# Performance work log

Measured on AMD Instinct MI355X. Metric: run time of the kernel, lower is better.

## Reference

```python
import jax, jax.numpy as jnp
import numpy as np

FP8_MAX = 448.0  # e4m3fn saturation value

def q8(x):
    """Round-to-nearest-even quantization to float8 e4m3fn values (kept in fp32).
    Normal min exponent -6, mantissa 3 bits, subnormal step 2^-9, saturate at 448."""
    a = jnp.abs(x)
    e = jnp.clip(jnp.floor(jnp.log2(jnp.maximum(a, 1e-30))), -6.0, 8.0)
    step = jnp.exp2(e - 3.0)  # mantissa quantization step for this binade
    q = jnp.minimum(jnp.round(a / step) * step, FP8_MAX)  # jnp.round is half-to-even
    return jnp.sign(x) * q

def setup_inputs() -> dict:
    key = jax.random.key(0)
    k1, k2, k3 = jax.random.split(key, 3)
    B, D_IN, D_H, D_OUT = 8192, 1024, 4096, 1024
    x = jax.random.normal(k1, (B, D_IN), jnp.float32)
    # learned weights (torch Linear layout: [out, in]); scaled to a realistic FP8 range
    w1 = jax.random.normal(k2, (D_H, D_IN), jnp.float32) * 0.03
    w2 = jax.random.normal(k3, (D_OUT, D_H), jnp.float32) * 0.03
    return {"x": x, "w1": w1, "w2": w2}

def reference(x, w1, w2):
    # x -> fp8 e4m3fn -> bit-pulse encode (lossless round trip for fp8 values)
    x8 = q8(x)
    # spike FP8 linear layers carry fp8 weights (set_weight_from_float quantizes)
    w1q = q8(w1)
    w2q = q8(w2)
    # fc1: spike spatial-encoding adder == accumulate wide, emit FP8 pulses
    h = q8(jnp.einsum('bi,hi->bh', x8, w1q))
    # SpikeFP8ReLU: zero out negative fp8 pulse values
    h = jnp.where(h > 0, h, 0.0)
    # fc2 then fp8_bits_to_float decode
    out = q8(jnp.einsum('bh,oh->bo', h, w2q))
    return out
```

## Files before the change

kernel.cpp:

```cpp
#include <hip/hip_runtime.h>
#include <stdint.h>
#include <stddef.h>

typedef int v4i  __attribute__((ext_vector_type(4)));
typedef int v16i __attribute__((ext_vector_type(16)));

#define KCH  256
#define BUFB (128 * 256)
#define LDSB (2 * BUFB)

__device__ __forceinline__ void gl_lds16(const uint8_t* g, uint8_t* l) {
    __builtin_amdgcn_global_load_lds(
        (const __attribute__((address_space(1))) uint32_t*)g,
        (__attribute__((address_space(3))) uint32_t*)l,
        16, 0, 0);
}

__device__ __forceinline__ float q8f(float v) {
    float a = fabsf(v);
    int e = (int)(__float_as_uint(a) >> 23) - 127;
    e = e < -6 ? -6 : (e > 8 ? 8 : e);
    float step  = __uint_as_float((uint32_t)(e - 3 + 127) << 23);
    float rstep = __uint_as_float((uint32_t)(3 - e + 127) << 23);
    float q = fminf(rintf(a * rstep) * step, 448.0f);
    return v < 0.0f ? -q : q;
}
__device__ __forceinline__ int qm(float v) {
    return (int)rintf(q8f(v) * 512.0f);
}

__device__ __forceinline__ uint32_t rne_sh(uint32_t a, int s) {
    uint32_t t = a >> s;
    uint32_t rem = a & ((1u << s) - 1u);
    uint32_t half = 1u << (s - 1);
    t += (rem > half) || (rem == half && (t & 1u));
    return t;
}

__global__ __launch_bounds__(256) void quant_all_kernel(
    const float* __restrict__ x,  uint8_t* __restrict__ xh, uint8_t* __restrict__ xl,
    const float* __restrict__ w1, uint32_t* __restrict__ w1m,
    const float* __restrict__ w2, uint32_t* __restrict__ w2m) {
    const int blk = blockIdx.x;
    const int tid = threadIdx.x;
    if (blk < 2048) {
        const int wave = tid >> 6, lane = tid & 63;
        const int rg = blk >> 3;
        const int g  = ((blk & 7) << 3) + wave * 2 + (lane >> 5);
        const int r  = rg * 32 + (lane & 31);
        const float* px = x + (size_t)r * 1024 + g * 16;
        v4i hv, lv;
#pragma unroll
        for (int q = 0; q < 4; ++q) {
            float4 v = ((const float4*)px)[q];
            int m0 = qm(v.x), m1 = qm(v.y), m2 = qm(v.z), m3 = qm(v.w);
            hv[q] = (int)(((uint32_t)((m0 >> 5) & 0xff)) | ((uint32_t)((m1 >> 5) & 0xff) << 8) |
                          ((uint32_t)((m2 >> 5) & 0xff) << 16) | ((uint32_t)((m3 >> 5) & 0xff) << 24));
            lv[q] = (int)(((uint32_t)(m0 & 31)) | ((uint32_t)(m1 & 31) << 8) |
                          ((uint32_t)(m2 & 31) << 16) | ((uint32_t)(m3 & 31) << 24));
        }
        const size_t pa = ((size_t)rg * 64 + g) * 512 + (size_t)(lane & 31) * 16;
        *(v4i*)(xh + pa) = hv;
        *(v4i*)(xl + pa) = lv;
    } else if (blk < 2048 + 4096) {
        int j = (blk - 2048) * 256 + tid;
        float4 v = ((const float4*)w1)[j];
        w1m[j] = ((uint32_t)(qm(v.x) & 0xff)) | ((uint32_t)(qm(v.y) & 0xff) << 8) |
                 ((uint32_t)(qm(v.z) & 0xff) << 16) | ((uint32_t)(qm(v.w) & 0xff) << 24);
    } else {
        int j = (blk - 6144) * 256 + tid;
        float4 v = ((const float4*)w2)[j];
        w2m[j] = ((uint32_t)(qm(v.x) & 0xff)) | ((uint32_t)(qm(v.y) & 0xff) << 8) |
                 ((uint32_t)(qm(v.z) & 0xff) << 16) | ((uint32_t)(qm(v.w) & 0xff) << 24);
    }
}

__device__ __forceinline__ void stage_chunk(
    const uint8_t* __restrict__ Bm, uint8_t* dst,
    int bn, int K, int kc, int wave, int lane) {
    const int r0 = lane >> 4;
    const int sl = lane & 15;
#pragma unroll
    for (int s = 0; s < 8; ++s) {
        const int qd  = wave * 8 + s;
        const int row = qd * 4 + r0;
        const int g   = sl ^ (row & 15);
        gl_lds16(Bm + (size_t)(bn * 128 + row) * K + kc + g * 16,
                 dst + qd * 1024 + lane * 16);
    }
}

template <int EPI>
__global__ __launch_bounds__(256, 2) void gemm_i8_big(
    const uint8_t* __restrict__ Ah, const uint8_t* __restrict__ Al,
    const uint8_t* __restrict__ Bm,
    void* __restrict__ Ch, void* __restrict__ Cl,
    int M, int N, int K) {
    extern __shared__ uint8_t sB[];

    const int tid  = threadIdx.x;
    const int lane = tid & 63;
    const int wave = tid >> 6;
    const int col  = lane & 31;
    const int kh   = lane >> 5;
    const int xm   = col & 15;

    const int bid = blockIdx.x;
    const int bm  = ((bid & 7) << 3) | ((bid >> 3) & 7);
    const int bn  = (((bid >> 9) << 3) | ((bid >> 6) & 7));

    v16i acc[2][4];
#pragma unroll
    for (int p = 0; p < 2; ++p)
#pragma unroll
        for (int j = 0; j < 4; ++j) acc[p][j] = (v16i)0;

    const size_t abase = (size_t)(bm * 4 + wave) * (K >> 4) * 512 + lane * 16;
    const uint8_t* pAh = Ah + abase;
    const uint8_t* pAl = Al + abase;

    int rowoff[4];
#pragma unroll
    for (int j = 0; j < 4; ++j) rowoff[j] = (j * 32 + col) * 256;

    const int NC = K / KCH;
    stage_chunk(Bm, sB, bn, K, 0, wave, lane);

    for (int c = 0; c < NC; ++c) {
        __syncthreads();
        const uint8_t* buf  = sB + (c & 1) * BUFB;
        const uint8_t* pAhc = pAh + (size_t)c * 8192;
        const uint8_t* pAlc = pAl + (size_t)c * 8192;

        v4i ab[8];
#pragma unroll
        for (int u = 0; u < 4; ++u) {
            ab[2 * u]     = *(const v4i*)(pAhc + u * 1024);
            ab[2 * u + 1] = *(const v4i*)(pAlc + u * 1024);
        }
        if (c + 1 < NC)
            stage_chunk(Bm, sB + ((c + 1) & 1) * BUFB, bn, K, (c + 1) * KCH, wave, lane);

#pragma unroll
        for (int u = 0; u < 4; ++u) {
            const int t = u;
            const int slot = ((2 * t + kh) & 15) ^ xm;
            v4i b[4];
#pragma unroll
            for (int j = 0; j < 4; ++j)
                b[j] = *(const v4i*)(buf + rowoff[j] + slot * 16);
#pragma unroll
            for (int j = 0; j < 4; ++j) {
                acc[0][j] = __builtin_amdgcn_mfma_i32_32x32x32_i8(ab[2 * u],     b[j], acc[0][j], 0, 0, 0);
                acc[1][j] = __builtin_amdgcn_mfma_i32_32x32x32_i8(ab[2 * u + 1], b[j], acc[1][j], 0, 0, 0);
            }
        }

#pragma unroll
        for (int u = 0; u < 4; ++u) {
            ab[2 * u]     = *(const v4i*)(pAhc + (4 + u) * 1024);
            ab[2 * u + 1] = *(const v4i*)(pAlc + (4 + u) * 1024);
        }

#pragma unroll
        for (int u = 0; u < 4; ++u) {
            const int t = 4 + u;
            const int slot = ((2 * t + kh) & 15) ^ xm;
            v4i b[4];
#pragma unroll
            for (int j = 0; j < 4; ++j)
                b[j] = *(const v4i*)(buf + rowoff[j] + slot * 16);
#pragma unroll
            for (int j = 0; j < 4; ++j) {
                acc[0][j] = __builtin_amdgcn_mfma_i32_32x32x32_i8(ab[2 * u],     b[j], acc[0][j], 0, 0, 0);
                acc[1][j] = __builtin_amdgcn_mfma_i32_32x32x32_i8(ab[2 * u + 1], b[j], acc[1][j], 0, 0, 0);
            }
        }
    }

    const int Gn = N >> 4;
    const int rb = bm * 4 + wave;
#pragma unroll
    for (int j = 0; j < 4; ++j) {
        const int colk = bn * 128 + j * 32 + col;
#pragma unroll
        for (int reg = 0; reg < 16; ++reg) {
            int mt = acc[0][j][reg] * 32 + acc[1][j][reg];
            const int rw = 4 * kh + (reg & 3) + 8 * (reg >> 2);
            if (EPI == 0) {
                uint8_t hb = 0, lb = 0;
                if (mt > 0) {
                    int s = 28 - __builtin_clz((uint32_t)mt);
                    if (s < 9) s = 9;
                    int mh = (int)(rne_sh((uint32_t)mt, s) << (s - 9));
                    hb = (uint8_t)(mh >> 5);
                    lb = (uint8_t)(mh & 31);
                }
                size_t pa = ((size_t)rb * Gn + (colk >> 4)) * 512 + rw * 16 + (colk & 15);
                ((uint8_t*)Ch)[pa] = hb;
                ((uint8_t*)Cl)[pa] = lb;
            } else {
                uint32_t a = mt < 0 ? (uint32_t)(-mt) : (uint32_t)mt;
                float v = 0.0f;
                if (a) {
                    int s = 28 - __builtin_clz(a);
                    if (s < 9) s = 9;
                    v = (float)(rne_sh(a, s) << s) * 0x1p-18f;
                    if (mt < 0) v = -v;
                }
                ((float*)Ch)[(size_t)(rb * 32 + rw) * N + colk] = v;
            }
        }
    }
}

extern "C" void kernel_launch(void* const* d_in, const int* in_sizes, int n_in,
                              void* d_out, int out_size, void* d_ws, size_t ws_size,
                              hipStream_t stream) {
    const int Bsz = 8192, DIN = 1024, DH = 4096, DOUT = 1024;
    const float* x  = (const float*)d_in[0];
    const float* w1 = (const float*)d_in[1];
    const float* w2 = (const float*)d_in[2];
    float* out = (float*)d_out;

    uint8_t* ws  = (uint8_t*)d_ws;
    uint8_t* xh  = ws;
    uint8_t* xl  = xh  + (size_t)Bsz * DIN;
    uint8_t* w1m = xl  + (size_t)Bsz * DIN;
    uint8_t* w2m = w1m + (size_t)DH  * DIN;
    uint8_t* hh  = w2m + (size_t)DOUT * DH;
    uint8_t* hl  = hh  + (size_t)Bsz * DH;

    static bool attr_done = false;
    if (!attr_done) {
        hipFuncSetAttribute((const void*)gemm_i8_big<0>,
                            hipFuncAttributeMaxDynamicSharedMemorySize, LDSB);
        hipFuncSetAttribute((const void*)gemm_i8_big<1>,
                            hipFuncAttributeMaxDynamicSharedMemorySize, LDSB);
        attr_done = true;
    }

    quant_all_kernel<<<10240, 256, 0, stream>>>(
        x, xh, xl, w1, (uint32_t*)w1m, w2, (uint32_t*)w2m);

    gemm_i8_big<0><<<dim3(2048), 256, LDSB, stream>>>(xh, xl, w1m, (void*)hh, (void*)hl, Bsz, DH, DIN);

    gemm_i8_big<1><<<dim3(512), 256, LDSB, stream>>>(hh, hl, w2m, (void*)out, nullptr, Bsz, DOUT, DH);
}
```

Measured before the change: 243.9 us.

## Pre-pack weights into MFMA fragment layout and load B directly from global

The quantization kernel now writes both weight matrices in the same packed 32-row fragment layout already used for activations. The GEMM drops the LDS double-buffer staging of B. Each wave instead loads its B fragments straight from global memory into registers, with one-step register prefetch of the next A and B fragments. This removes the LDS traffic, barriers and shared-memory limit, at the cost of every wave re-reading B from global/L2 instead of sharing it through LDS.

```diff
diff --git a/kernel.cpp b/kernel.cpp
--- a/kernel.cpp
+++ b/kernel.cpp
@@ -4,17 +4,6 @@
 
 typedef int v4i  __attribute__((ext_vector_type(4)));
 typedef int v16i __attribute__((ext_vector_type(16)));
-
-#define KCH  256
-#define BUFB (128 * 256)
-#define LDSB (2 * BUFB)
-
-__device__ __forceinline__ void gl_lds16(const uint8_t* g, uint8_t* l) {
-    __builtin_amdgcn_global_load_lds(
-        (const __attribute__((address_space(1))) uint32_t*)g,
-        (__attribute__((address_space(3))) uint32_t*)l,
-        16, 0, 0);
-}
 
 __device__ __forceinline__ float q8f(float v) {
     float a = fabsf(v);
@@ -39,16 +28,17 @@
 
 __global__ __launch_bounds__(256) void quant_all_kernel(
     const float* __restrict__ x,  uint8_t* __restrict__ xh, uint8_t* __restrict__ xl,
-    const float* __restrict__ w1, uint32_t* __restrict__ w1m,
-    const float* __restrict__ w2, uint32_t* __restrict__ w2m) {
+    const float* __restrict__ w1, uint8_t* __restrict__ w1p,
+    const float* __restrict__ w2, uint8_t* __restrict__ w2p) {
     const int blk = blockIdx.x;
     const int tid = threadIdx.x;
+    const int wave = tid >> 6, lane = tid & 63;
+    const int gsub = wave * 2 + (lane >> 5);
+    const int rr = lane & 31;
     if (blk < 2048) {
-        const int wave = tid >> 6, lane = tid & 63;
         const int rg = blk >> 3;
-        const int g  = ((blk & 7) << 3) + wave * 2 + (lane >> 5);
-        const int r  = rg * 32 + (lane & 31);
-        const float* px = x + (size_t)r * 1024 + g * 16;
+        const int g  = ((blk & 7) << 3) + gsub;
+        const float* px = x + (size_t)(rg * 32 + rr) * 1024 + g * 16;
         v4i hv, lv;
 #pragma unroll
         for (int q = 0; q < 4; ++q) {
@@ -59,51 +49,49 @@
             lv[q] = (int)(((uint32_t)(m0 & 31)) | ((uint32_t)(m1 & 31) << 8) |
                           ((uint32_t)(m2 & 31) << 16) | ((uint32_t)(m3 & 31) << 24));
         }
-        const size_t pa = ((size_t)rg * 64 + g) * 512 + (size_t)(lane & 31) * 16;
+        const size_t pa = ((size_t)rg * 64 + g) * 512 + (size_t)rr * 16;
         *(v4i*)(xh + pa) = hv;
         *(v4i*)(xl + pa) = lv;
-    } else if (blk < 2048 + 4096) {
-        int j = (blk - 2048) * 256 + tid;
-        float4 v = ((const float4*)w1)[j];
-        w1m[j] = ((uint32_t)(qm(v.x) & 0xff)) | ((uint32_t)(qm(v.y) & 0xff) << 8) |
-                 ((uint32_t)(qm(v.z) & 0xff) << 16) | ((uint32_t)(qm(v.w) & 0xff) << 24);
+    } else if (blk < 3072) {
+        const int j  = blk - 2048;
+        const int rg = j >> 3;
+        const int g  = ((j & 7) << 3) + gsub;
+        const float* pw = w1 + (size_t)(rg * 32 + rr) * 1024 + g * 16;
+        v4i bv;
+#pragma unroll
+        for (int q = 0; q < 4; ++q) {
+            float4 v = ((const float4*)pw)[q];
+            bv[q] = (int)(((uint32_t)(qm(v.x) & 0xff)) | ((uint32_t)(qm(v.y) & 0xff) << 8) |
+                          ((uint32_t)(qm(v.z) & 0xff) << 16) | ((uint32_t)(qm(v.w) & 0xff) << 24));
+        }
+        *(v4i*)(w1p + ((size_t)rg * 64 + g) * 512 + (size_t)rr * 16) = bv;
     } else {
-        int j = (blk - 6144) * 256 + tid;
-        float4 v = ((const float4*)w2)[j];
-        w2m[j] = ((uint32_t)(qm(v.x) & 0xff)) | ((uint32_t)(qm(v.y) & 0xff) << 8) |
-                 ((uint32_t)(qm(v.z) & 0xff) << 16) | ((uint32_t)(qm(v.w) & 0xff) << 24);
-    }
-}
-
-__device__ __forceinline__ void stage_chunk(
-    const uint8_t* __restrict__ Bm, uint8_t* dst,
-    int bn, int K, int kc, int wave, int lane) {
-    const int r0 = lane >> 4;
-    const int sl = lane & 15;
-#pragma unroll
-    for (int s = 0; s < 8; ++s) {
-        const int qd  = wave * 8 + s;
-        const int row = qd * 4 + r0;
-        const int g   = sl ^ (row & 15);
-        gl_lds16(Bm + (size_t)(bn * 128 + row) * K + kc + g * 16,
-                 dst + qd * 1024 + lane * 16);
+        const int j  = blk - 3072;
+        const int rg = j >> 5;
+        const int g  = ((j & 31) << 3) + gsub;
+        const float* pw = w2 + (size_t)(rg * 32 + rr) * 4096 + g * 16;
+        v4i bv;
+#pragma unroll
+        for (int q = 0; q < 4; ++q) {
+            float4 v = ((const float4*)pw)[q];
+            bv[q] = (int)(((uint32_t)(qm(v.x) & 0xff)) | ((uint32_t)(qm(v.y) & 0xff) << 8) |
+                          ((uint32_t)(qm(v.z) & 0xff) << 16) | ((uint32_t)(qm(v.w) & 0xff) << 24));
+        }
+        *(v4i*)(w2p + ((size_t)rg * 256 + g) * 512 + (size_t)rr * 16) = bv;
     }
 }
 
 template <int EPI>
 __global__ __launch_bounds__(256, 2) void gemm_i8_big(
     const uint8_t* __restrict__ Ah, const uint8_t* __restrict__ Al,
-    const uint8_t* __restrict__ Bm,
+    const uint8_t* __restrict__ Bp,
     void* __restrict__ Ch, void* __restrict__ Cl,
     int M, int N, int K) {
-    extern __shared__ uint8_t sB[];
-
     const int tid  = threadIdx.x;
     const int lane = tid & 63;
     const int wave = tid >> 6;
     const int col  = lane & 31;
     const int kh   = lane >> 5;
-    const int xm   = col & 15;
 
     const int bid = blockIdx.x;
     const int bm  = ((bid & 7) << 3) | ((bid >> 3) & 7);
@@ -115,67 +103,47 @@
 #pragma unroll
         for (int j = 0; j < 4; ++j) acc[p][j] = (v16i)0;
 
-    const size_t abase = (size_t)(bm * 4 + wave) * (K >> 4) * 512 + lane * 16;
-    const uint8_t* pAh = Ah + abase;
-    const uint8_t* pAl = Al + abase;
-
-    int rowoff[4];
-#pragma unroll
-    for (int j = 0; j < 4; ++j) rowoff[j] = (j * 32 + col) * 256;
-
-    const int NC = K / KCH;
-    stage_chunk(Bm, sB, bn, K, 0, wave, lane);
-
-    for (int c = 0; c < NC; ++c) {
-        __syncthreads();
-        const uint8_t* buf  = sB + (c & 1) * BUFB;
-        const uint8_t* pAhc = pAh + (size_t)c * 8192;
-        const uint8_t* pAlc = pAl + (size_t)c * 8192;
-
-        v4i ab[8];
+    const size_t gstride = (size_t)(K >> 4) * 512;
+    const uint8_t* pAh = Ah + (size_t)(bm * 4 + wave) * gstride + lane * 16;
+    const uint8_t* pAl = Al + (size_t)(bm * 4 + wave) * gstride + lane * 16;
+    const uint8_t* pB  = Bp + (size_t)(bn * 4) * gstride + lane * 16;
+
+    const int NT = K >> 5;
+    const int NG = NT >> 2;
+
+    v4i ab[8], abn[8], bc[4], bn_[4];
+#pragma unroll
+    for (int u = 0; u < 4; ++u) {
+        ab[2 * u]     = *(const v4i*)(pAh + u * 1024);
+        ab[2 * u + 1] = *(const v4i*)(pAl + u * 1024);
+    }
+#pragma unroll
+    for (int j = 0; j < 4; ++j) bc[j] = *(const v4i*)(pB + j * gstride);
+
+    for (int g = 0; g < NG; ++g) {
+        __builtin_amdgcn_s_barrier();
+        const int gn = (g + 1 < NG) ? (g + 1) : g;
+        const uint8_t* pAhn = pAh + (size_t)gn * 4096;
+        const uint8_t* pAln = pAl + (size_t)gn * 4096;
 #pragma unroll
         for (int u = 0; u < 4; ++u) {
-            ab[2 * u]     = *(const v4i*)(pAhc + u * 1024);
-            ab[2 * u + 1] = *(const v4i*)(pAlc + u * 1024);
-        }
-        if (c + 1 < NC)
-            stage_chunk(Bm, sB + ((c + 1) & 1) * BUFB, bn, K, (c + 1) * KCH, wave, lane);
-
-#pragma unroll
-        for (int u = 0; u < 4; ++u) {
-            const int t = u;
-            const int slot = ((2 * t + kh) & 15) ^ xm;
-            v4i b[4];
+            const int t  = g * 4 + u;
+            const int tn = (t + 1 < NT) ? (t + 1) : t;
 #pragma unroll
             for (int j = 0; j < 4; ++j)
-                b[j] = *(const v4i*)(buf + rowoff[j] + slot * 16);
+                bn_[j] = *(const v4i*)(pB + j * gstride + (size_t)tn * 1024);
+            abn[2 * u]     = *(const v4i*)(pAhn + u * 1024);
+            abn[2 * u + 1] = *(const v4i*)(pAln + u * 1024);
 #pragma unroll
             for (int j = 0; j < 4; ++j) {
-                acc[0][j] = __builtin_amdgcn_mfma_i32_32x32x32_i8(ab[2 * u],     b[j], acc[0][j], 0, 0, 0);
-                acc[1][j] = __builtin_amdgcn_mfma_i32_32x32x32_i8(ab[2 * u + 1], b[j], acc[1][j], 0, 0, 0);
+                acc[0][j] = __builtin_amdgcn_mfma_i32_32x32x32_i8(ab[2 * u],     bc[j], acc[0][j], 0, 0, 0);
+                acc[1][j] = __builtin_amdgcn_mfma_i32_32x32x32_i8(ab[2 * u + 1], bc[j], acc[1][j], 0, 0, 0);
             }
-        }
-
-#pragma unroll
-        for (int u = 0; u < 4; ++u) {
-            ab[2 * u]     = *(const v4i*)(pAhc + (4 + u) * 1024);
-            ab[2 * u + 1] = *(const v4i*)(pAlc + (4 + u) * 1024);
-        }
-
-#pragma unroll
-        for (int u = 0; u < 4; ++u) {
-            const int t = 4 + u;
-            const int slot = ((2 * t + kh) & 15) ^ xm;
-            v4i b[4];
-#pragma unroll
-            for (int j = 0; j < 4; ++j)
-                b[j] = *(const v4i*)(buf + rowoff[j] + slot * 16);
-#pragma unroll
-            for (int j = 0; j < 4; ++j) {
-                acc[0][j] = __builtin_amdgcn_mfma_i32_32x32x32_i8(ab[2 * u],     b[j], acc[0][j], 0, 0, 0);
-                acc[1][j] = __builtin_amdgcn_mfma_i32_32x32x32_i8(ab[2 * u + 1], b[j], acc[1][j], 0, 0, 0);
-            }
-        }
+#pragma unroll
+            for (int j = 0; j < 4; ++j) bc[j] = bn_[j];
+        }
+#pragma unroll
+        for (int r = 0; r < 8; ++r) ab[r] = abn[r];
     }
 
     const int Gn = N >> 4;
@@ -226,24 +194,14 @@
     uint8_t* ws  = (uint8_t*)d_ws;
     uint8_t* xh  = ws;
     uint8_t* xl  = xh  + (size_t)Bsz * DIN;
-    uint8_t* w1m = xl  + (size_t)Bsz * DIN;
-    uint8_t* w2m = w1m + (size_t)DH  * DIN;
-    uint8_t* hh  = w2m + (size_t)DOUT * DH;
+    uint8_t* w1p = xl  + (size_t)Bsz * DIN;
+    uint8_t* w2p = w1p + (size_t)DH  * DIN;
+    uint8_t* hh  = w2p + (size_t)DOUT * DH;
     uint8_t* hl  = hh  + (size_t)Bsz * DH;
 
-    static bool attr_done = false;
-    if (!attr_done) {
-        hipFuncSetAttribute((const void*)gemm_i8_big<0>,
-                            hipFuncAttributeMaxDynamicSharedMemorySize, LDSB);
-        hipFuncSetAttribute((const void*)gemm_i8_big<1>,
-                            hipFuncAttributeMaxDynamicSharedMemorySize, LDSB);
-        attr_done = true;
-    }
-
-    quant_all_kernel<<<10240, 256, 0, stream>>>(
-        x, xh, xl, w1, (uint32_t*)w1m, w2, (uint32_t*)w2m);
-
-    gemm_i8_big<0><<<dim3(2048), 256, LDSB, stream>>>(xh, xl, w1m, (void*)hh, (void*)hl, Bsz, DH, DIN);
-
-    gemm_i8_big<1><<<dim3(512), 256, LDSB, stream>>>(hh, hl, w2m, (void*)out, nullptr, Bsz, DOUT, DH);
-}
+    quant_all_kernel<<<4096, 256, 0, stream>>>(x, xh, xl, w1, w1p, w2, w2p);
+
+    gemm_i8_big<0><<<dim3(2048), 256, 0, stream>>>(xh, xl, w1p, (void*)hh, (void*)hl, Bsz, DH, DIN);
+
+    gemm_i8_big<1><<<dim3(512), 256, 0, stream>>>(hh, hl, w2p, (void*)out, nullptr, Bsz, DOUT, DH);
+}
```

Result: slower. 396.4 us (+62.5%).

## Prefetch A fragments one stage ahead and use raw barrier with MFMA priority

Applied to the files above, without the earlier changes.

The A-operand register loads are restructured into a two-buffer software pipeline. The first half-chunk of A is loaded before the loop, and each half is prefetched while the MFMAs for the previous half run, so global load latency is hidden behind compute. `__syncthreads` is replaced by a bare `s_barrier` with compiler fences, and MFMA blocks are wrapped in `s_setprio` to favour the matrix work. The bare barrier no longer waits for outstanding global-to-LDS loads from other waves, so correctness now depends on the ordering of vmcnt waits. The extra A registers also raise register pressure.

```diff
diff --git a/kernel.cpp b/kernel.cpp
--- a/kernel.cpp
+++ b/kernel.cpp
@@ -8,6 +8,8 @@
 #define KCH  256
 #define BUFB (128 * 256)
 #define LDSB (2 * BUFB)
+
+#define FENCE() asm volatile("" ::: "memory")
 
 __device__ __forceinline__ void gl_lds16(const uint8_t* g, uint8_t* l) {
     __builtin_amdgcn_global_load_lds(
@@ -124,58 +126,77 @@
     for (int j = 0; j < 4; ++j) rowoff[j] = (j * 32 + col) * 256;
 
     const int NC = K / KCH;
+
     stage_chunk(Bm, sB, bn, K, 0, wave, lane);
+    FENCE();
+    v4i a0[8], a1[8];
+#pragma unroll
+    for (int u = 0; u < 4; ++u) {
+        a0[2 * u]     = *(const v4i*)(pAh + u * 1024);
+        a0[2 * u + 1] = *(const v4i*)(pAl + u * 1024);
+    }
+    FENCE();
+    asm volatile("s_waitcnt vmcnt(8)" ::: "memory");
 
     for (int c = 0; c < NC; ++c) {
-        __syncthreads();
+        __builtin_amdgcn_s_barrier();
+        FENCE();
         const uint8_t* buf  = sB + (c & 1) * BUFB;
         const uint8_t* pAhc = pAh + (size_t)c * 8192;
         const uint8_t* pAlc = pAl + (size_t)c * 8192;
 
-        v4i ab[8];
-#pragma unroll
-        for (int u = 0; u < 4; ++u) {
-            ab[2 * u]     = *(const v4i*)(pAhc + u * 1024);
-            ab[2 * u + 1] = *(const v4i*)(pAlc + u * 1024);
-        }
         if (c + 1 < NC)
             stage_chunk(Bm, sB + ((c + 1) & 1) * BUFB, bn, K, (c + 1) * KCH, wave, lane);
-
+        FENCE();
 #pragma unroll
         for (int u = 0; u < 4; ++u) {
-            const int t = u;
-            const int slot = ((2 * t + kh) & 15) ^ xm;
+            a1[2 * u]     = *(const v4i*)(pAhc + (4 + u) * 1024);
+            a1[2 * u + 1] = *(const v4i*)(pAlc + (4 + u) * 1024);
+        }
+        FENCE();
+
+#pragma unroll
+        for (int u = 0; u < 4; ++u) {
+            const int slot = ((2 * u + kh) & 15) ^ xm;
             v4i b[4];
 #pragma unroll
             for (int j = 0; j < 4; ++j)
                 b[j] = *(const v4i*)(buf + rowoff[j] + slot * 16);
+            __builtin_amdgcn_s_setprio(1);
 #pragma unroll
             for (int j = 0; j < 4; ++j) {
-                acc[0][j] = __builtin_amdgcn_mfma_i32_32x32x32_i8(ab[2 * u],     b[j], acc[0][j], 0, 0, 0);
-                acc[1][j] = __builtin_amdgcn_mfma_i32_32x32x32_i8(ab[2 * u + 1], b[j], acc[1][j], 0, 0, 0);
-            }
-        }
+                acc[0][j] = __builtin_amdgcn_mfma_i32_32x32x32_i8(a0[2 * u],     b[j], acc[0][j], 0, 0, 0);
+                acc[1][j] = __builtin_amdgcn_mfma_i32_32x32x32_i8(a0[2 * u + 1], b[j], acc[1][j], 0, 0, 0);
+            }
+            __builtin_amdgcn_s_setprio(0);
+        }
+        FENCE();
+
+        if (c + 1 < NC) {
+#pragma unroll
+            for (int u = 0; u < 4; ++u) {
+                a0[2 * u]     = *(const v4i*)(pAhc + 8192 + u * 1024);
+                a0[2 * u + 1] = *(const v4i*)(pAlc + 8192 + u * 1024);
+            }
+        }
+        FENCE();
 
 #pragma unroll
         for (int u = 0; u < 4; ++u) {
-            ab[2 * u]     = *(const v4i*)(pAhc + (4 + u) * 1024);
-            ab[2 * u + 1] = *(const v4i*)(pAlc + (4 + u) * 1024);
-        }
-
-#pragma unroll
-        for (int u = 0; u < 4; ++u) {
-            const int t = 4 + u;
-            const int slot = ((2 * t + kh) & 15) ^ xm;
+            const int slot = ((2 * (4 + u) + kh) & 15) ^ xm;
             v4i b[4];
 #pragma unroll
             for (int j = 0; j < 4; ++j)
                 b[j] = *(const v4i*)(buf + rowoff[j] + slot * 16);
+            __builtin_amdgcn_s_setprio(1);
 #pragma unroll
             for (int j = 0; j < 4; ++j) {
-                acc[0][j] = __builtin_amdgcn_mfma_i32_32x32x32_i8(ab[2 * u],     b[j], acc[0][j], 0, 0, 0);
-                acc[1][j] = __builtin_amdgcn_mfma_i32_32x32x32_i8(ab[2 * u + 1], b[j], acc[1][j], 0, 0, 0);
-            }
-        }
+                acc[0][j] = __builtin_amdgcn_mfma_i32_32x32x32_i8(a1[2 * u],     b[j], acc[0][j], 0, 0, 0);
+                acc[1][j] = __builtin_amdgcn_mfma_i32_32x32x32_i8(a1[2 * u + 1], b[j], acc[1][j], 0, 0, 0);
+            }
+            __builtin_amdgcn_s_setprio(0);
+        }
+        FENCE();
     }
 
     const int Gn = N >> 4;
```

Result: slower. 276.5 us (+13.4%).

## Software-pipeline A-fragment loads and interleave B staging with MFMA phases

Applied to the files above, without the earlier changes.

Restructures the GEMM main loop so the A-operand global loads for the next pair of k-steps are issued one phase ahead, and the next chunk's B staging into LDS is split into four pieces spread across the compute phases. The full __syncthreads is replaced by explicit waitcnt plus s_barrier with sched barriers, and the MFMA groups run at raised wave priority. The aim is to hide global load latency behind MFMA work rather than stalling at the top of each chunk. The hand-placed vmcnt counts are fragile and could be wrong for this load count. The one-time guard on the function attribute calls is also removed, adding host calls on every launch.

```diff
diff --git a/kernel.cpp b/kernel.cpp
--- a/kernel.cpp
+++ b/kernel.cpp
@@ -8,6 +8,8 @@
 #define KCH  256
 #define BUFB (128 * 256)
 #define LDSB (2 * BUFB)
+
+#define FENCE() asm volatile("" ::: "memory")
 
 __device__ __forceinline__ void gl_lds16(const uint8_t* g, uint8_t* l) {
     __builtin_amdgcn_global_load_lds(
@@ -90,6 +92,21 @@
     }
 }
 
+__device__ __forceinline__ void stage_pair(
+    const uint8_t* __restrict__ Bm, uint8_t* dst,
+    int bn, int K, int kc, int wave, int lane, int p) {
+    const int r0 = lane >> 4;
+    const int sl = lane & 15;
+#pragma unroll
+    for (int s = 2 * p; s < 2 * p + 2; ++s) {
+        const int qd  = wave * 8 + s;
+        const int row = qd * 4 + r0;
+        const int g   = sl ^ (row & 15);
+        gl_lds16(Bm + (size_t)(bn * 128 + row) * K + kc + g * 16,
+                 dst + qd * 1024 + lane * 16);
+    }
+}
+
 template <int EPI>
 __global__ __launch_bounds__(256, 2) void gemm_i8_big(
     const uint8_t* __restrict__ Ah, const uint8_t* __restrict__ Al,
@@ -124,58 +141,69 @@
     for (int j = 0; j < 4; ++j) rowoff[j] = (j * 32 + col) * 256;
 
     const int NC = K / KCH;
+
     stage_chunk(Bm, sB, bn, K, 0, wave, lane);
+    FENCE();
+    v4i aC0 = *(const v4i*)(pAh);
+    v4i aC1 = *(const v4i*)(pAl);
+    v4i aC2 = *(const v4i*)(pAh + 1024);
+    v4i aC3 = *(const v4i*)(pAl + 1024);
+    FENCE();
+    asm volatile("s_waitcnt vmcnt(4)" ::: "memory");
+    __builtin_amdgcn_sched_barrier(0);
 
     for (int c = 0; c < NC; ++c) {
-        __syncthreads();
+        asm volatile("s_waitcnt lgkmcnt(0)" ::: "memory");
+        __builtin_amdgcn_sched_barrier(0);
+        __builtin_amdgcn_s_barrier();
+        FENCE();
         const uint8_t* buf  = sB + (c & 1) * BUFB;
+        uint8_t*       nbuf = sB + ((c + 1) & 1) * BUFB;
+        const bool  more    = (c + 1 < NC);
+        const int   nkc     = (c + 1) * KCH;
         const uint8_t* pAhc = pAh + (size_t)c * 8192;
         const uint8_t* pAlc = pAl + (size_t)c * 8192;
-
-        v4i ab[8];
-#pragma unroll
-        for (int u = 0; u < 4; ++u) {
-            ab[2 * u]     = *(const v4i*)(pAhc + u * 1024);
-            ab[2 * u + 1] = *(const v4i*)(pAlc + u * 1024);
+        const size_t next_off = more ? 8192 : 0;
+
+#pragma unroll
+        for (int p = 0; p < 4; ++p) {
+            if (more) stage_pair(Bm, nbuf, bn, K, nkc, wave, lane, p);
+            FENCE();
+            const size_t tb = (p == 3) ? next_off : (size_t)(2 * p + 2) * 1024;
+            v4i aN0 = *(const v4i*)(pAhc + tb);
+            v4i aN1 = *(const v4i*)(pAlc + tb);
+            v4i aN2 = *(const v4i*)(pAhc + tb + 1024);
+            v4i aN3 = *(const v4i*)(pAlc + tb + 1024);
+            FENCE();
+#pragma unroll
+            for (int e = 0; e < 2; ++e) {
+                const int t = 2 * p + e;
+                const int slot = ((2 * t + kh) & 15) ^ xm;
+                v4i b[4];
+#pragma unroll
+                for (int j = 0; j < 4; ++j)
+                    b[j] = *(const v4i*)(buf + rowoff[j] + slot * 16);
+                __builtin_amdgcn_s_setprio(1);
+                if (e == 0) {
+#pragma unroll
+                    for (int j = 0; j < 4; ++j) {
+                        acc[0][j] = __builtin_amdgcn_mfma_i32_32x32x32_i8(aC0, b[j], acc[0][j], 0, 0, 0);
+                        acc[1][j] = __builtin_amdgcn_mfma_i32_32x32x32_i8(aC1, b[j], acc[1][j], 0, 0, 0);
+                    }
+                } else {
+#pragma unroll
+                    for (int j = 0; j < 4; ++j) {
+                        acc[0][j] = __builtin_amdgcn_mfma_i32_32x32x32_i8(aC2, b[j], acc[0][j], 0, 0, 0);
+                        acc[1][j] = __builtin_amdgcn_mfma_i32_32x32x32_i8(aC3, b[j], acc[1][j], 0, 0, 0);
+                    }
+                }
+                __builtin_amdgcn_s_setprio(0);
+            }
+            FENCE();
+            aC0 = aN0; aC1 = aN1; aC2 = aN2; aC3 = aN3;
         }
-        if (c + 1 < NC)
-            stage_chunk(Bm, sB + ((c + 1) & 1) * BUFB, bn, K, (c + 1) * KCH, wave, lane);
-
-#pragma unroll
-        for (int u = 0; u < 4; ++u) {
-            const int t = u;
-            const int slot = ((2 * t + kh) & 15) ^ xm;
-            v4i b[4];
-#pragma unroll
-            for (int j = 0; j < 4; ++j)
-                b[j] = *(const v4i*)(buf + rowoff[j] + slot * 16);
-#pragma unroll
-            for (int j = 0; j < 4; ++j) {
-                acc[0][j] = __builtin_amdgcn_mfma_i32_32x32x32_i8(ab[2 * u],     b[j], acc[0][j], 0, 0, 0);
-                acc[1][j] = __builtin_amdgcn_mfma_i32_32x32x32_i8(ab[2 * u + 1], b[j], acc[1][j], 0, 0, 0);
-            }
-        }
-
-#pragma unroll
-        for (int u = 0; u < 4; ++u) {
-            ab[2 * u]     = *(const v4i*)(pAhc + (4 + u) * 1024);
-            ab[2 * u + 1] = *(const v4i*)(pAlc + (4 + u) * 1024);
-        }
-
-#pragma unroll
-        for (int u = 0; u < 4; ++u) {
-            const int t = 4 + u;
-            const int slot = ((2 * t + kh) & 15) ^ xm;
-            v4i b[4];
-#pragma unroll
-            for (int j = 0; j < 4; ++j)
-                b[j] = *(const v4i*)(buf + rowoff[j] + slot * 16);
-#pragma unroll
-            for (int j = 0; j < 4; ++j) {
-                acc[0][j] = __builtin_amdgcn_mfma_i32_32x32x32_i8(ab[2 * u],     b[j], acc[0][j], 0, 0, 0);
-                acc[1][j] = __builtin_amdgcn_mfma_i32_32x32x32_i8(ab[2 * u + 1], b[j], acc[1][j], 0, 0, 0);
-            }
-        }
+        asm volatile("s_waitcnt vmcnt(4)" ::: "memory");
+        __builtin_amdgcn_sched_barrier(0);
     }
 
     const int Gn = N >> 4;
@@ -231,14 +259,10 @@
     uint8_t* hh  = w2m + (size_t)DOUT * DH;
     uint8_t* hl  = hh  + (size_t)Bsz * DH;
 
-    static bool attr_done = false;
-    if (!attr_done) {
-        hipFuncSetAttribute((const void*)gemm_i8_big<0>,
-                            hipFuncAttributeMaxDynamicSharedMemorySize, LDSB);
-        hipFuncSetAttribute((const void*)gemm_i8_big<1>,
-                            hipFuncAttributeMaxDynamicSharedMemorySize, LDSB);
-        attr_done = true;
-    }
+    hipFuncSetAttribute((const void*)gemm_i8_big<0>,
+                        hipFuncAttributeMaxDynamicSharedMemorySize, LDSB);
+    hipFuncSetAttribute((const void*)gemm_i8_big<1>,
+                        hipFuncAttributeMaxDynamicSharedMemorySize, LDSB);
 
     quant_all_kernel<<<10240, 256, 0, stream>>>(
         x, xh, xl, w1, (uint32_t*)w1m, w2, (uint32_t*)w2m);
```

Result: no change. 244.6 us (+0.3%).
